# Performance work log

Hardware: AMD Instinct MI355X
Metric: run time of the kernel (lower is better)

The kernel has to match this reference:

```python
import jax, jax.numpy as jnp
import numpy as np

O, I, KH, KW = 256, 128, 3, 3
STRIDE, PADDING, DILATION, GROUPS = (1, 1), (1, 1), (1, 1), 1


def setup_inputs() -> dict:
    key = jax.random.key(0)
    kx, kw, kb = jax.random.split(key, 3)
    x = jax.random.normal(kx, (16, I, 112, 112), dtype=jnp.float32)
    # Build a realistic float weight, then quantize+pack exactly like the torch module.
    W = jax.random.normal(kw, (O, I, KH, KW), dtype=jnp.float32) * 0.05
    min_val = jnp.min(W)
    max_val = jnp.max(W)
    scale = (max_val - min_val) / 255.0
    q = jnp.clip(jnp.round((W - min_val) / scale), 0, 255).astype(jnp.uint8).reshape(-1)
    q1 = q[0::2].astype(jnp.float16)
    q2 = q[1::2].astype(jnp.float16)
    # torch promotion: fp16 / fp32 -> fp32, fp16 + fp32 -> fp32, so buffer is fp32
    packed_weight = q1.astype(jnp.float32) + q2.astype(jnp.float32) / jnp.float32(255.0)
    bias = jax.random.normal(kb, (O,), dtype=jnp.float32) * 0.1
    return {
        "x": x,
        "packed_weight": packed_weight,
        "scale_w": scale.astype(jnp.float32),
        "zero_point": min_val.astype(jnp.float32),
        "bias": bias,
    }


def _unpack_weights(packed_weight, scale_w, zero_point):
    q1 = jnp.floor(packed_weight)                       # first code of each pair
    q2 = jnp.clip(jnp.round((packed_weight - q1) * 255.0), 0.0, 255.0)
    # interleave q1, q2 back into the flat code stream
    q = jnp.stack([q1, q2], axis=-1).reshape(-1)        # [O*I*KH*KW]
    w = q.reshape(O, I, KH, KW).astype(jnp.float16)     # torch casts to fp16 here
    return w.astype(jnp.float32) * scale_w + zero_point


def reference(x, packed_weight, scale_w, zero_point, bias):
    w = _unpack_weights(packed_weight, scale_w, zero_point)
    out = jax.lax.conv_general_dilated(
        x, w,
        window_strides=STRIDE,
        padding=[(PADDING[0], PADDING[0]), (PADDING[1], PADDING[1])],
        rhs_dilation=DILATION,
        dimension_numbers=("NCHW", "OIHW", "NCHW"),
        feature_group_count=GROUPS,
    )
    return out + bias[None, :, None, None]
```

## Files before the change

### kernel.cpp

```cpp
#include <hip/hip_runtime.h>


#define C_IN  128
#define H_IN  112
#define W_IN  112
#define HW    (H_IN * W_IN)
#define N_B   16
#define O_C   256
#define P_TOT (N_B * HW)

#define HP    114
#define XP_OFF   (1u << 20)
#define XP_BYTES (16u * 114u * 114u * 128u * 2u)
#define WS_NEED  (XP_OFF + XP_BYTES)

typedef __attribute__((ext_vector_type(8))) short bhalf8;
typedef __attribute__((ext_vector_type(4))) float floatx4;

__device__ __forceinline__ unsigned short f2bf(float f) {
  union { float f; unsigned u; } v; v.f = f;
  return (unsigned short)((v.u + 0x7FFFu + ((v.u >> 16) & 1u)) >> 16);
}

#define GLL16(srcp, ldsp)                                                     \
  __builtin_amdgcn_global_load_lds(                                           \
      (const __attribute__((address_space(1))) unsigned int*)(srcp),          \
      (__attribute__((address_space(3))) unsigned int*)(ldsp), 16, 0, 0)


__global__ void dequant_fast(const float* __restrict__ pw,
                             const float* __restrict__ scale_p,
                             const float* __restrict__ zp_p,
                             unsigned short* __restrict__ Wd) {
  int i = blockIdx.x * 256 + threadIdx.x;
  if (i >= (O_C * C_IN * 9) / 2) return;
  float p = pw[i];
  float s = scale_p[0], z = zp_p[0];
  float q1 = floorf(p);
  float q2 = rintf((p - q1) * 255.0f);
  q2 = fminf(fmaxf(q2, 0.0f), 255.0f);
  float wv[2] = { q1 * s + z, q2 * s + z };
#pragma unroll
  for (int k = 0; k < 2; ++k) {
    int f = 2 * i + k;
    int o = f / 1152;
    int rem = f - o * 1152;
    int c = rem / 9;
    int r = rem - c * 9;
    Wd[((r * 16 + (c >> 3)) * 256 + o) * 8 + (c & 7)] = f2bf(wv[k]);
  }
}

__global__ void zero_border(unsigned short* __restrict__ xp) {
  int idx = blockIdx.x * 256 + threadIdx.x;
  if (idx >= N_B * 452 * 16) return;
  int n   = idx / (452 * 16);
  int rem = idx - n * (452 * 16);
  int b   = rem >> 4;
  int c8  = rem & 15;
  int h, w;
  if      (b < 114) { h = 0;           w = b; }
  else if (b < 228) { h = 113;         w = b - 114; }
  else if (b < 340) { h = b - 228 + 1; w = 0; }
  else              { h = b - 340 + 1; w = 113; }
  bhalf8 z = {0, 0, 0, 0, 0, 0, 0, 0};
  *(bhalf8*)(xp + ((size_t)(n * HP + h) * HP + w) * 128 + c8 * 8) = z;
}

__global__ void pad_kernel(const float* __restrict__ x,
                           unsigned short* __restrict__ xp) {
  __shared__ unsigned short sh[128][60];
  const int tid = threadIdx.x;
  const int s = blockIdx.x;
  const int h = blockIdx.y;
  const int n = blockIdx.z;
  const int w0 = s * 56;

#pragma unroll
  for (int k = 0; k < 7; ++k) {
    int idx = tid + 256 * k;
    int c = idx / 14;
    int wq = idx - c * 14;
    const float* src = x + (size_t)(n * 128 + c) * HW + h * W_IN + w0 + wq * 4;
    float4 v = *(const float4*)src;
    ushort4 b;
    b.x = f2bf(v.x); b.y = f2bf(v.y); b.z = f2bf(v.z); b.w = f2bf(v.w);
    *(ushort4*)&sh[c][wq * 4] = b;
  }
  __syncthreads();
#pragma unroll
  for (int k = 0; k < 4; ++k) {
    int idx = tid + 256 * k;
    if (idx < 896) {
      int wl = idx >> 4, c8 = idx & 15;
      bhalf8 v;
#pragma unroll
      for (int j = 0; j < 8; ++j) v[j] = (short)sh[c8 * 8 + j][wl];
      unsigned short* dst = xp +
          ((size_t)(n * HP + h + 1) * HP + (w0 + wl + 1)) * 128 + c8 * 8;
      *(bhalf8*)dst = v;
    }
  }
}


__global__ __launch_bounds__(512, 2) void conv_fast(
    const unsigned short* __restrict__ xp,
    const unsigned short* __restrict__ Wd,
    const float* __restrict__ bias,
    float* __restrict__ out)
{
  __shared__ unsigned short As[3 * 4 * 256 * 8];
  __shared__ unsigned short Bs[3 * 4 * 128 * 8];

  const int tid  = threadIdx.x;
  const int lane = tid & 63;
  const int wave = tid >> 6;
  const int wm   = wave >> 1;
  const int wn   = wave & 1;
  const int lr   = lane >> 4;
  const int lc   = lane & 15;

  const int bswz = (blockIdx.x & 7) * 196 + (blockIdx.x >> 3);
  const int p0  = bswz * 128;
  const int n   = p0 / HW;
  const int hw0 = p0 - n * HW;

  const int pp  = tid & 127;
  const int hwp = hw0 + pp;
  const int h   = hwp / W_IN;
  const int w   = hwp - h * W_IN;
  const unsigned short* bsrc =
      xp + ((size_t)(n * HP + h + 1) * HP + (w + 1)) * 128 + (tid >> 7) * 8;

  const unsigned short* asrc = Wd + tid * 8;

  unsigned short* adst = As + wave * 512;
  unsigned short* bdst = Bs + wave * 512;

  const unsigned short* arow = As + lr * 2048 + (wm * 64 + lc) * 8;
  const unsigned short* brow = Bs + lr * 1024 + (wn * 64 + lc) * 8;

  floatx4 acc[4][4];
#pragma unroll
  for (int a = 0; a < 4; ++a)
#pragma unroll
    for (int b = 0; b < 4; ++b)
      acc[a][b] = (floatx4){0.f, 0.f, 0.f, 0.f};

  auto stageA = [&](int t, int buf) {
    int r = t >> 2, q4 = t & 3;
    const unsigned short* s = asrc + (r * 16 + q4 * 4) * 2048;
    GLL16(s,        adst + buf * 8192);
    GLL16(s + 4096, adst + buf * 8192 + 4096);
  };
  auto stageB = [&](int t, int buf) {
    int r = t >> 2, q4 = t & 3;
    int dh = r / 3, dw = r - dh * 3;
    int tap = (dh - 1) * HP + (dw - 1);
    GLL16(bsrc + tap * 128 + q4 * 32, bdst + buf * 4096);
  };

  stageA(0, 0); stageB(0, 0);
  stageA(1, 1); stageB(1, 1);
  asm volatile("s_waitcnt vmcnt(3)" ::: "memory");
  __builtin_amdgcn_s_barrier();

  int buf = 0;
  for (int kt = 0; kt < 34; ++kt) {
    int sbuf = buf + 2; if (sbuf >= 3) sbuf -= 3;
    const unsigned short* ar = arow + buf * 8192;
    const unsigned short* br = brow + buf * 4096;
    bhalf8 af[4], bfv[4];

#pragma unroll
    for (int mi = 0; mi < 4; ++mi) af[mi] = *(const bhalf8*)(ar + mi * 128);
#pragma unroll
    for (int ni = 0; ni < 4; ++ni) bfv[ni] = *(const bhalf8*)(br + ni * 128);
    stageA(kt + 2, sbuf);
    stageB(kt + 2, sbuf);
    __builtin_amdgcn_s_barrier();
    asm volatile("s_waitcnt lgkmcnt(0)" ::: "memory");
    __builtin_amdgcn_sched_barrier(0);
    __builtin_amdgcn_s_setprio(1);
#pragma unroll
    for (int mi = 0; mi < 4; ++mi)
#pragma unroll
      for (int ni = 0; ni < 4; ++ni)
        acc[mi][ni] = __builtin_amdgcn_mfma_f32_16x16x32_bf16(
            af[mi], bfv[ni], acc[mi][ni], 0, 0, 0);
    __builtin_amdgcn_s_setprio(0);
    asm volatile("s_waitcnt vmcnt(3)" ::: "memory");
    __builtin_amdgcn_s_barrier();

    buf = (buf + 1 == 3) ? 0 : buf + 1;
  }

  asm volatile("s_waitcnt vmcnt(0)" ::: "memory");
  __builtin_amdgcn_s_barrier();
#pragma unroll
  for (int kk = 0; kk < 2; ++kk) {
    int b2 = (34 + kk) % 3;
    const unsigned short* ar = arow + b2 * 8192;
    const unsigned short* br = brow + b2 * 4096;
    bhalf8 af[4], bfv[4];
#pragma unroll
    for (int mi = 0; mi < 4; ++mi) af[mi]  = *(const bhalf8*)(ar + mi * 128);
#pragma unroll
    for (int ni = 0; ni < 4; ++ni) bfv[ni] = *(const bhalf8*)(br + ni * 128);
#pragma unroll
    for (int mi = 0; mi < 4; ++mi)
#pragma unroll
      for (int ni = 0; ni < 4; ++ni)
        acc[mi][ni] = __builtin_amdgcn_mfma_f32_16x16x32_bf16(
            af[mi], bfv[ni], acc[mi][ni], 0, 0, 0);
  }

#pragma unroll
  for (int mi = 0; mi < 4; ++mi) {
#pragma unroll
    for (int j = 0; j < 4; ++j) {
      const int o  = wm * 64 + mi * 16 + lr * 4 + j;
      const float bo = bias[o];
      float* orow = out + ((size_t)(n * O_C + o)) * HW + hw0 + wn * 64;
#pragma unroll
      for (int ni = 0; ni < 4; ++ni)
        orow[ni * 16 + lc] = acc[mi][ni][j] + bo;
    }
  }
}


__global__ void dequant_kernel(const float* __restrict__ pw,
                               const float* __restrict__ scale_p,
                               const float* __restrict__ zp_p,
                               unsigned short* __restrict__ Wd) {
  int i = blockIdx.x * 256 + threadIdx.x;
  if (i >= (O_C * C_IN * 9) / 2) return;
  float p = pw[i];
  float s = scale_p[0], z = zp_p[0];
  float q1 = floorf(p);
  float q2 = rintf((p - q1) * 255.0f);
  q2 = fminf(fmaxf(q2, 0.0f), 255.0f);
  float wv[2] = { q1 * s + z, q2 * s + z };
#pragma unroll
  for (int k = 0; k < 2; ++k) {
    int f = 2 * i + k;
    int o = f / 1152;
    int rem = f - o * 1152;
    int c = rem / 9;
    int r = rem - c * 9;
    Wd[(r * O_C + o) * C_IN + c] = f2bf(wv[k]);
  }
}

__global__ __launch_bounds__(256, 2) void conv_kernel(
    const float* __restrict__ x,
    const unsigned short* __restrict__ Wd,
    const float* __restrict__ bias,
    float* __restrict__ out)
{
  __shared__ unsigned short As[128][32];
  __shared__ unsigned short Bs[4][128][8];
  const int tid  = threadIdx.x;
  const int lane = tid & 63;
  const int wave = tid >> 6;
  const int wm   = wave >> 1;
  const int wn   = wave & 1;
  const int p0   = blockIdx.x * 128;
  const int o0   = blockIdx.y * 128;
  const int n    = p0 / HW;
  const int hw0  = p0 - n * HW;
  const int pp = tid & 127;
  const int qh = tid >> 7;
  const int hwp = hw0 + pp;
  const int h  = hwp / W_IN;
  const int w  = hwp - h * W_IN;
  const int xnbase = n * C_IN * HW;
  const int lr = lane >> 4;
  const int lc = lane & 15;
  floatx4 acc[4][4];
#pragma unroll
  for (int a = 0; a < 4; ++a)
#pragma unroll
    for (int b = 0; b < 4; ++b)
      acc[a][b] = (floatx4){0.f, 0.f, 0.f, 0.f};
  for (int r = 0; r < 9; ++r) {
    const int dh = r / 3 - 1;
    const int dw = r % 3 - 1;
    const int ih = h + dh;
    const int iw = w + dw;
    const bool valid = ((unsigned)ih < (unsigned)H_IN) & ((unsigned)iw < (unsigned)W_IN);
    const int xb = xnbase + ih * W_IN + iw;
    const unsigned short* Wr = Wd + r * (O_C * C_IN);
    for (int c0 = 0; c0 < C_IN; c0 += 32) {
      __syncthreads();
#pragma unroll
      for (int j = 0; j < 2; ++j) {
        int sdx  = tid + 256 * j;
        int oo = sdx >> 2;
        int c8 = (sdx & 3) << 3;
        bhalf8 v = *(const bhalf8*)(Wr + (o0 + oo) * C_IN + c0 + c8);
        *(bhalf8*)(&As[oo][c8]) = v;
      }
#pragma unroll
      for (int j = 0; j < 2; ++j) {
        int q = qh + 2 * j;
        bhalf8 v;
        if (valid) {
          const float* xpp = x + xb + (c0 + (q << 3)) * HW;
#pragma unroll
          for (int i = 0; i < 8; ++i) v[i] = (short)f2bf(xpp[i * HW]);
        } else {
#pragma unroll
          for (int i = 0; i < 8; ++i) v[i] = 0;
        }
        *(bhalf8*)(&Bs[q][pp][0]) = v;
      }
      __syncthreads();
      bhalf8 af[4], bfv[4];
#pragma unroll
      for (int mi = 0; mi < 4; ++mi)
        af[mi] = *(const bhalf8*)(&As[wm * 64 + mi * 16 + lc][lr << 3]);
#pragma unroll
      for (int ni = 0; ni < 4; ++ni)
        bfv[ni] = *(const bhalf8*)(&Bs[lr][wn * 64 + ni * 16 + lc][0]);
#pragma unroll
      for (int mi = 0; mi < 4; ++mi)
#pragma unroll
        for (int ni = 0; ni < 4; ++ni)
          acc[mi][ni] = __builtin_amdgcn_mfma_f32_16x16x32_bf16(
              af[mi], bfv[ni], acc[mi][ni], 0, 0, 0);
    }
  }
#pragma unroll
  for (int mi = 0; mi < 4; ++mi) {
#pragma unroll
    for (int j = 0; j < 4; ++j) {
      const int o  = o0 + wm * 64 + mi * 16 + lr * 4 + j;
      const float bo = bias[o];
      float* orow = out + (n * O_C + o) * HW + hw0 + wn * 64;
#pragma unroll
      for (int ni = 0; ni < 4; ++ni)
        orow[ni * 16 + lc] = acc[mi][ni][j] + bo;
    }
  }
}


extern "C" void kernel_launch(void* const* d_in, const int* in_sizes, int n_in,
                              void* d_out, int out_size, void* d_ws, size_t ws_size,
                              hipStream_t stream) {
  const float* x    = (const float*)d_in[0];
  const float* pw   = (const float*)d_in[1];
  const float* sw   = (const float*)d_in[2];
  const float* zp   = (const float*)d_in[3];
  const float* bias = (const float*)d_in[4];
  float* out = (float*)d_out;
  unsigned short* Wd = (unsigned short*)d_ws;

  if (ws_size >= WS_NEED) {
    unsigned short* xp = (unsigned short*)((char*)d_ws + XP_OFF);
    dequant_fast<<<dim3((O_C * C_IN * 9 / 2 + 255) / 256), dim3(256), 0, stream>>>(
        pw, sw, zp, Wd);
    zero_border<<<dim3((N_B * 452 * 16 + 255) / 256), dim3(256), 0, stream>>>(xp);
    pad_kernel<<<dim3(2, H_IN, N_B), dim3(256), 0, stream>>>(x, xp);
    conv_fast<<<dim3(P_TOT / 128), dim3(512), 0, stream>>>(xp, Wd, bias, out);
  } else {
    dequant_kernel<<<dim3((O_C * C_IN * 9 / 2 + 255) / 256), dim3(256), 0, stream>>>(
        pw, sw, zp, Wd);
    dim3 grid(P_TOT / 128, O_C / 128);
    conv_kernel<<<grid, dim3(256), 0, stream>>>(x, Wd, bias, out);
  }
}
```

Measured before the change: 179.2 us.

## Load weight fragments directly from global into registers, drop A LDS staging

Weight (A) tiles are no longer staged through shared memory. Each lane now loads its MFMA fragments directly from global memory into registers, prefetched one k-step ahead, and only the activation tile still uses the triple-buffered LDS pipeline. This removes the A LDS traffic and one barrier per iteration and shrinks LDS use, and launch bounds are raised to target 4 blocks per CU. The risks are exposed global/L2 latency on the weight loads, since only one step is prefetched, and register pressure from the higher occupancy target.

```diff
diff --git a/kernel.cpp b/kernel.cpp
--- a/kernel.cpp
+++ b/kernel.cpp
@@ -104,13 +104,12 @@
 }
 
 
-__global__ __launch_bounds__(512, 2) void conv_fast(
+__global__ __launch_bounds__(512, 4) void conv_fast(
     const unsigned short* __restrict__ xp,
     const unsigned short* __restrict__ Wd,
     const float* __restrict__ bias,
     float* __restrict__ out)
 {
-  __shared__ unsigned short As[3 * 4 * 256 * 8];
   __shared__ unsigned short Bs[3 * 4 * 128 * 8];
 
   const int tid  = threadIdx.x;
@@ -133,12 +132,10 @@
   const unsigned short* bsrc =
       xp + ((size_t)(n * HP + h + 1) * HP + (w + 1)) * 128 + (tid >> 7) * 8;
 
-  const unsigned short* asrc = Wd + tid * 8;
-
-  unsigned short* adst = As + wave * 512;
+  const unsigned short* agbase = Wd + ((size_t)lr * 256 + wm * 64 + lc) * 8;
+
   unsigned short* bdst = Bs + wave * 512;
 
-  const unsigned short* arow = As + lr * 2048 + (wm * 64 + lc) * 8;
   const unsigned short* brow = Bs + lr * 1024 + (wn * 64 + lc) * 8;
 
   floatx4 acc[4][4];
@@ -148,12 +145,6 @@
     for (int b = 0; b < 4; ++b)
       acc[a][b] = (floatx4){0.f, 0.f, 0.f, 0.f};
 
-  auto stageA = [&](int t, int buf) {
-    int r = t >> 2, q4 = t & 3;
-    const unsigned short* s = asrc + (r * 16 + q4 * 4) * 2048;
-    GLL16(s,        adst + buf * 8192);
-    GLL16(s + 4096, adst + buf * 8192 + 4096);
-  };
   auto stageB = [&](int t, int buf) {
     int r = t >> 2, q4 = t & 3;
     int dh = r / 3, dw = r - dh * 3;
@@ -161,26 +152,27 @@
     GLL16(bsrc + tap * 128 + q4 * 32, bdst + buf * 4096);
   };
 
-  stageA(0, 0); stageB(0, 0);
-  stageA(1, 1); stageB(1, 1);
-  asm volatile("s_waitcnt vmcnt(3)" ::: "memory");
+  bhalf8 a[4];
+
+  stageB(0, 0);
+  stageB(1, 1);
+#pragma unroll
+  for (int mi = 0; mi < 4; ++mi)
+    a[mi] = *(const bhalf8*)(agbase + mi * 128);
+  asm volatile("s_waitcnt vmcnt(5)" ::: "memory");
   __builtin_amdgcn_s_barrier();
 
   int buf = 0;
   for (int kt = 0; kt < 34; ++kt) {
     int sbuf = buf + 2; if (sbuf >= 3) sbuf -= 3;
-    const unsigned short* ar = arow + buf * 8192;
     const unsigned short* br = brow + buf * 4096;
-    bhalf8 af[4], bfv[4];
-
-#pragma unroll
-    for (int mi = 0; mi < 4; ++mi) af[mi] = *(const bhalf8*)(ar + mi * 128);
+    bhalf8 bfv[4];
+
 #pragma unroll
     for (int ni = 0; ni < 4; ++ni) bfv[ni] = *(const bhalf8*)(br + ni * 128);
-    stageA(kt + 2, sbuf);
     stageB(kt + 2, sbuf);
-    __builtin_amdgcn_s_barrier();
     asm volatile("s_waitcnt lgkmcnt(0)" ::: "memory");
+    asm volatile("s_waitcnt vmcnt(1)" ::: "memory");
     __builtin_amdgcn_sched_barrier(0);
     __builtin_amdgcn_s_setprio(1);
 #pragma unroll
@@ -188,32 +180,59 @@
 #pragma unroll
       for (int ni = 0; ni < 4; ++ni)
         acc[mi][ni] = __builtin_amdgcn_mfma_f32_16x16x32_bf16(
-            af[mi], bfv[ni], acc[mi][ni], 0, 0, 0);
+            a[mi], bfv[ni], acc[mi][ni], 0, 0, 0);
     __builtin_amdgcn_s_setprio(0);
-    asm volatile("s_waitcnt vmcnt(3)" ::: "memory");
+    {
+      const unsigned short* ag = agbase + (size_t)(kt + 1) * 8192;
+#pragma unroll
+      for (int mi = 0; mi < 4; ++mi)
+        a[mi] = *(const bhalf8*)(ag + mi * 128);
+    }
     __builtin_amdgcn_s_barrier();
 
     buf = (buf + 1 == 3) ? 0 : buf + 1;
   }
 
-  asm volatile("s_waitcnt vmcnt(0)" ::: "memory");
-  __builtin_amdgcn_s_barrier();
-#pragma unroll
-  for (int kk = 0; kk < 2; ++kk) {
-    int b2 = (34 + kk) % 3;
-    const unsigned short* ar = arow + b2 * 8192;
-    const unsigned short* br = brow + b2 * 4096;
-    bhalf8 af[4], bfv[4];
-#pragma unroll
-    for (int mi = 0; mi < 4; ++mi) af[mi]  = *(const bhalf8*)(ar + mi * 128);
+  {
+    const unsigned short* br = brow + buf * 4096;
+    bhalf8 bfv[4];
 #pragma unroll
     for (int ni = 0; ni < 4; ++ni) bfv[ni] = *(const bhalf8*)(br + ni * 128);
+    asm volatile("s_waitcnt lgkmcnt(0)" ::: "memory");
+    asm volatile("s_waitcnt vmcnt(0)" ::: "memory");
+    __builtin_amdgcn_sched_barrier(0);
+    __builtin_amdgcn_s_setprio(1);
 #pragma unroll
     for (int mi = 0; mi < 4; ++mi)
 #pragma unroll
       for (int ni = 0; ni < 4; ++ni)
         acc[mi][ni] = __builtin_amdgcn_mfma_f32_16x16x32_bf16(
-            af[mi], bfv[ni], acc[mi][ni], 0, 0, 0);
+            a[mi], bfv[ni], acc[mi][ni], 0, 0, 0);
+    __builtin_amdgcn_s_setprio(0);
+    {
+      const unsigned short* ag = agbase + (size_t)35 * 8192;
+#pragma unroll
+      for (int mi = 0; mi < 4; ++mi)
+        a[mi] = *(const bhalf8*)(ag + mi * 128);
+    }
+    __builtin_amdgcn_s_barrier();
+    buf = (buf + 1 == 3) ? 0 : buf + 1;
+  }
+
+  {
+    const unsigned short* br = brow + buf * 4096;
+    bhalf8 bfv[4];
+#pragma unroll
+    for (int ni = 0; ni < 4; ++ni) bfv[ni] = *(const bhalf8*)(br + ni * 128);
+    asm volatile("s_waitcnt lgkmcnt(0)" ::: "memory");
+    asm volatile("s_waitcnt vmcnt(0)" ::: "memory");
+    __builtin_amdgcn_sched_barrier(0);
+#pragma unroll
+    for (int mi = 0; mi < 4; ++mi)
+#pragma unroll
+      for (int ni = 0; ni < 4; ++ni)
+        acc[mi][ni] = __builtin_amdgcn_mfma_f32_16x16x32_bf16(
+            a[mi], bfv[ni], acc[mi][ni], 0, 0, 0);
   }
 
 #pragma unroll
```

After: 197.7 us. 1.1x slower.
